# Kernel tuning notes

Hardware: AMD Instinct MI355X
Metric: run time of the kernel (lower is better)

Reference implementation:

```python
import jax, jax.numpy as jnp
import numpy as np

H, C = 16, 5           # GAT heads, per-head out channels
SIZE = 500             # max_pool_x size (time bins)
GAT_SLOPE, ACT_SLOPE = 0.2, 0.01


def _lrelu(x, s):
    return jnp.where(x >= 0, x, s * x)


def _gat(x, src, dst, ea, mask, W, We, a_s, a_d, a_e, b):
    # PyG GATConv: shared src/dst lin, edge_dim, self-loops already appended by caller
    N = x.shape[0]
    xp = (x @ W.T).reshape(N, H, C)                                   # [N,H,C]
    al = (jnp.einsum('nhc,hc->nh', xp, a_s)[src]
          + jnp.einsum('nhc,hc->nh', xp, a_d)[dst]
          + jnp.einsum('ehc,hc->eh', (ea @ We.T).reshape(-1, H, C), a_e))  # [E,H]
    al = _lrelu(al, GAT_SLOPE)
    if mask is not None:  # masked-out edges contribute nothing (equivalent to edge removal)
        al = jnp.where(mask[:, None], al, -jnp.inf)
    m = jax.ops.segment_max(al, dst, num_segments=N)                  # finite: every node has a self-loop
    e = jnp.exp(al - m[dst])
    coef = e / jax.ops.segment_sum(e, dst, num_segments=N)[dst]       # segment softmax over incoming edges
    out = jax.ops.segment_sum(coef[:, :, None] * xp[src], dst, num_segments=N)
    return out.reshape(N, H * C) + b


def _conv(x, w, b):
    y = jax.lax.conv_general_dilated(x, w, (2,), [(1, 1)],
                                     dimension_numbers=('NCH', 'OIH', 'NCH'))
    return y + b[None, :, None]


def _mlp(z, w1, b1, w2, b2, w3, b3):
    z = _lrelu(z @ w1.T + b1, ACT_SLOPE)
    z = _lrelu(z @ w2.T + b2, ACT_SLOPE)
    return z @ w3.T + b3


def _forward(x, edge_attr,
             gat1_W, gat1_We, gat1_as, gat1_ad, gat1_ae, gat1_b,
             gat2_W, gat2_We, gat2_as, gat2_ad, gat2_ae, gat2_b,
             conv1_w, conv1_b, conv2_w, conv2_b, conv3_w, conv3_b,
             chi_w1, chi_b1, chi_w2, chi_b2, chi_w3, chi_b3,
             rp_w1, rp_b1, rp_w2, rp_b2, rp_w3, rp_b3,
             t0_w1, t0_b1, t0_w2, t0_b2, t0_w3, t0_b3,
             edge_index, num_graphs):
    N = x.shape[0]
    loops = jnp.arange(N, dtype=edge_index.dtype)
    src = jnp.concatenate([edge_index[0], loops])
    dst = jnp.concatenate([edge_index[1], loops])
    ea = jnp.concatenate([edge_attr, jnp.zeros((N, edge_attr.shape[1]), edge_attr.dtype)], axis=0)
    timing = x[:, 2].astype(jnp.int32)   # non-differentiable, like .to(torch.long)

    h = _gat(x, src, dst, ea, None, gat1_W, gat1_We, gat1_as, gat1_ad, gat1_ae, gat1_b)
    mask2 = jnp.concatenate([edge_attr[:, 0] > 1.0, jnp.ones((N,), bool)])  # EdgeV[:,0]>1 + self loops
    h = _gat(h, src, dst, ea, mask2, gat2_W, gat2_We, gat2_as, gat2_ad, gat2_ae, gat2_b)

    # max_pool_x(cluster=Timing, batch, size=500): scatter-max into B*500 slots,
    # empty slots -> 0 (torch_scatter semantics); then view(-1, 80, 500)
    pooled = jax.ops.segment_max(h, timing, num_segments=num_graphs * SIZE)
    pooled = jnp.where(jnp.isfinite(pooled), pooled, 0.0)
    z = pooled.reshape(num_graphs, H * C, SIZE)

    z = _lrelu(_conv(z, conv1_w, conv1_b), ACT_SLOPE)   # [B,16,247]
    z = _lrelu(_conv(z, conv2_w, conv2_b), ACT_SLOPE)   # [B,16,120]
    z = _lrelu(_conv(z, conv3_w, conv3_b), ACT_SLOPE)   # [B,16,57]
    L = z.shape[-1]
    nw = (L - 10) // 10 + 1                              # MaxPool1d(k=10,s=10) -> 5
    z = z[..., :nw * 10].reshape(z.shape[0], z.shape[1], nw, 10).max(-1)
    z = z.reshape(z.shape[0], -1)                        # [B,80]

    chi0 = jnp.tanh(_mlp(z, chi_w1, chi_b1, chi_w2, chi_b2, chi_w3, chi_b3))
    rp = _mlp(z, rp_w1, rp_b1, rp_w2, rp_b2, rp_w3, rp_b3)
    t0 = _mlp(z, t0_w1, t0_b1, t0_w2, t0_b2, t0_w3, t0_b3)
    return jnp.concatenate([chi0, rp, t0], axis=1)       # [B,3]


def setup_inputs() -> dict:
    key = jax.random.key(0)
    ki = iter(jax.random.split(key, 50))
    N, E, B = 100_000, 1_200_000, 64
    x = jax.random.normal(next(ki), (N, 5), jnp.float32)
    timing = jax.random.randint(next(ki), (N,), 0, SIZE)
    x = x.at[:, 2].set(timing.astype(jnp.float32))       # Timing column holds integer bins
    src = jax.random.randint(next(ki), (E,), 0, N, dtype=jnp.int32)
    off = jax.random.randint(next(ki), (E,), 1, N, dtype=jnp.int32)
    dst = (src + off) % N                                # no pre-existing self-loops (PyG strips them)
    edge_index = jnp.stack([src, dst])
    edge_attr = jax.random.uniform(next(ki), (E, 2), jnp.float32) * 3.0  # ~2/3 pass col0>1 mask
    batch = jnp.sort(jax.random.randint(next(ki), (N,), 0, B, dtype=jnp.int32))

    def p(shape, scale=0.1):
        return jax.random.normal(next(ki), shape, jnp.float32) * scale

    return dict(
        x=x, edge_attr=edge_attr,
        gat1_W=p((80, 5)), gat1_We=p((80, 2)), gat1_as=p((16, 5)), gat1_ad=p((16, 5)), gat1_ae=p((16, 5)), gat1_b=p((80,)),
        gat2_W=p((80, 80)), gat2_We=p((80, 2)), gat2_as=p((16, 5)), gat2_ad=p((16, 5)), gat2_ae=p((16, 5)), gat2_b=p((80,)),
        conv1_w=p((16, 80, 10)), conv1_b=p((16,)),
        conv2_w=p((16, 16, 10)), conv2_b=p((16,)),
        conv3_w=p((16, 16, 10)), conv3_b=p((16,)),
        chi_w1=p((128, 80)), chi_b1=p((128,)), chi_w2=p((128, 128)), chi_b2=p((128,)), chi_w3=p((1, 128)), chi_b3=p((1,)),
        rp_w1=p((128, 80)), rp_b1=p((128,)), rp_w2=p((128, 128)), rp_b2=p((128,)), rp_w3=p((1, 128)), rp_b3=p((1,)),
        t0_w1=p((128, 80)), t0_b1=p((128,)), t0_w2=p((128, 128)), t0_b2=p((128,)), t0_w3=p((1, 128)), t0_b3=p((1,)),
        edge_index=edge_index, batch=batch, num_graphs=B)


def reference(x, edge_attr,
              gat1_W, gat1_We, gat1_as, gat1_ad, gat1_ae, gat1_b,
              gat2_W, gat2_We, gat2_as, gat2_ad, gat2_ae, gat2_b,
              conv1_w, conv1_b, conv2_w, conv2_b, conv3_w, conv3_b,
              chi_w1, chi_b1, chi_w2, chi_b2, chi_w3, chi_b3,
              rp_w1, rp_b1, rp_w2, rp_b2, rp_w3, rp_b3,
              t0_w1, t0_b1, t0_w2, t0_b2, t0_w3, t0_b3,
              edge_index, batch, num_graphs):
    del batch  # only used in torch to compute batch_size (passed here as num_graphs)
    return _forward(x, edge_attr,
                    gat1_W, gat1_We, gat1_as, gat1_ad, gat1_ae, gat1_b,
                    gat2_W, gat2_We, gat2_as, gat2_ad, gat2_ae, gat2_b,
                    conv1_w, conv1_b, conv2_w, conv2_b, conv3_w, conv3_b,
                    chi_w1, chi_b1, chi_w2, chi_b2, chi_w3, chi_b3,
                    rp_w1, rp_b1, rp_w2, rp_b2, rp_w3, rp_b3,
                    t0_w1, t0_b1, t0_w2, t0_b2, t0_w3, t0_b3,
                    edge_index, num_graphs)
```

## Files before the change

### kernel.cpp

```cpp
#include <hip/hip_runtime.h>
#include <math.h>

#define DEV static __device__ __forceinline__

DEV unsigned fenc(float f) {
    unsigned u = __float_as_uint(f);
    return (u & 0x80000000u) ? ~u : (u | 0x80000000u);
}
DEV float fdec(unsigned u) {
    return __uint_as_float((u & 0x80000000u) ? (u ^ 0x80000000u) : ~u);
}
DEV void atomic_max_u32(unsigned* p, unsigned v) {
    __hip_atomic_fetch_max(p, v, __ATOMIC_RELAXED, __HIP_MEMORY_SCOPE_AGENT);
}
DEV unsigned bf16(float f) {
    unsigned u = __float_as_uint(f);
    return (u + 0x7FFFu + ((u >> 16) & 1u)) >> 16;
}
DEV float unbf16(unsigned s) { return __uint_as_float(s << 16); }

__global__ void k_proj5t(const float* __restrict__ x, const float* __restrict__ W,
                         const float* __restrict__ a_s, const float* __restrict__ a_d,
                         unsigned short* __restrict__ xpb, float* __restrict__ dterm, int N) {
    int i = blockIdx.x * blockDim.x + threadIdx.x;
    if (i >= N * 16) return;
    int n = i >> 4, h = i & 15;
    float xr[5];
    #pragma unroll
    for (int j = 0; j < 5; ++j) xr[j] = x[(size_t)n * 5 + j];
    float o[5];
    #pragma unroll
    for (int c = 0; c < 5; ++c) {
        const float* wr = W + (size_t)(h * 5 + c) * 5;
        float s = 0.f;
        #pragma unroll
        for (int j = 0; j < 5; ++j) s += xr[j] * wr[j];
        o[c] = s;
    }
    float ss = 0.f, sd = 0.f;
    #pragma unroll
    for (int c = 0; c < 5; ++c) { ss += o[c] * a_s[h * 5 + c]; sd += o[c] * a_d[h * 5 + c]; }
    unsigned* p = (unsigned*)(xpb + (size_t)n * 96 + h * 6);
    p[0] = bf16(o[0]) | (bf16(o[1]) << 16);
    p[1] = bf16(o[2]) | (bf16(o[3]) << 16);
    p[2] = bf16(o[4]) | (bf16(ss) << 16);
    dterm[i] = sd;
}

__global__ __launch_bounds__(256) void k_proj80t(
    const unsigned short* __restrict__ in,
    const float* __restrict__ W,
    const float* __restrict__ a_s, const float* __restrict__ a_d,
    unsigned short* __restrict__ xpb, float* __restrict__ dterm, int N) {
    __shared__ float XS[16 * 136];
    __shared__ float WS[16 * 81];
    int tid = threadIdx.x;
    int n0 = blockIdx.x * 128;
    int h = tid & 15, ng = tid >> 4;

    float acc[8][5];
    #pragma unroll
    for (int j = 0; j < 8; ++j)
        #pragma unroll
        for (int c = 0; c < 5; ++c) acc[j][c] = 0.f;

    for (int k0 = 0; k0 < 80; k0 += 16) {
        __syncthreads();
        {
            int r = tid >> 1;
            int halfk = (tid & 1) * 8;
            int n = n0 + r; if (n >= N) n = N - 1;
            const uint4 v = *(const uint4*)(in + (size_t)n * 80 + k0 + halfk);
            unsigned uu[4] = {v.x, v.y, v.z, v.w};
            #pragma unroll
            for (int j = 0; j < 4; ++j) {
                XS[(halfk + 2 * j)     * 136 + r] = unbf16(uu[j] & 0xffff);
                XS[(halfk + 2 * j + 1) * 136 + r] = unbf16(uu[j] >> 16);
            }
        }
        {
            #pragma unroll
            for (int i = 0; i < 5; ++i) {
                int j = tid + i * 256;
                int oc = j >> 4, kk = j & 15;
                WS[kk * 81 + oc] = W[(size_t)oc * 80 + k0 + kk];
            }
        }
        __syncthreads();
        #pragma unroll
        for (int kk = 0; kk < 16; ++kk) {
            float4 xa = *(const float4*)&XS[kk * 136 + ng * 8];
            float4 xb = *(const float4*)&XS[kk * 136 + ng * 8 + 4];
            float wv[5];
            #pragma unroll
            for (int c = 0; c < 5; ++c) wv[c] = WS[kk * 81 + h * 5 + c];
            float xv[8] = {xa.x, xa.y, xa.z, xa.w, xb.x, xb.y, xb.z, xb.w};
            #pragma unroll
            for (int j = 0; j < 8; ++j)
                #pragma unroll
                for (int c = 0; c < 5; ++c) acc[j][c] += xv[j] * wv[c];
        }
    }
    float as_[5], ad_[5];
    #pragma unroll
    for (int c = 0; c < 5; ++c) { as_[c] = a_s[h * 5 + c]; ad_[c] = a_d[h * 5 + c]; }
    #pragma unroll
    for (int j = 0; j < 8; ++j) {
        int n = n0 + ng * 8 + j;
        if (n < N) {
            float ss = 0.f, sd = 0.f;
            #pragma unroll
            for (int c = 0; c < 5; ++c) { ss += acc[j][c] * as_[c]; sd += acc[j][c] * ad_[c]; }
            unsigned* p = (unsigned*)(xpb + (size_t)n * 96 + h * 6);
            p[0] = bf16(acc[j][0]) | (bf16(acc[j][1]) << 16);
            p[1] = bf16(acc[j][2]) | (bf16(acc[j][3]) << 16);
            p[2] = bf16(acc[j][4]) | (bf16(ss) << 16);
            dterm[n * 16 + h] = sd;
        }
    }
}

#define BIN_TILE 4096
__global__ __launch_bounds__(256) void k_cnt512(const int* __restrict__ dst,
        int* __restrict__ bcnt, int E, int NB) {
    __shared__ int cnt[512];
    int tid = threadIdx.x;
    for (int b = tid; b < NB; b += 256) cnt[b] = 0;
    __syncthreads();
    int e0 = blockIdx.x * BIN_TILE;
    #pragma unroll
    for (int k = 0; k < BIN_TILE / 256; ++k) {
        int e = e0 + k * 256 + tid;
        if (e < E) atomicAdd(&cnt[((unsigned)dst[e]) >> 8], 1);
    }
    __syncthreads();
    for (int b = tid; b < NB; b += 256) {
        int c = cnt[b];
        if (c) __hip_atomic_fetch_add(&bcnt[b], c, __ATOMIC_RELAXED, __HIP_MEMORY_SCOPE_AGENT);
    }
}

__global__ void k_scan512(const int* __restrict__ bcnt, int* __restrict__ boff,
                          int* __restrict__ bcur, int* __restrict__ off,
                          int NB, int N, int E) {
    __shared__ int sm[512];
    int t = threadIdx.x;
    int v = (t < NB) ? bcnt[t] : 0;
    sm[t] = v;
    __syncthreads();
    for (int s = 1; s < 512; s <<= 1) {
        int u = (t >= s) ? sm[t - s] : 0;
        __syncthreads();
        sm[t] += u;
        __syncthreads();
    }
    int excl = sm[t] - v;
    if (t < NB) { boff[t] = excl; bcur[t] = excl; }
    if (t == NB - 1) boff[NB] = excl + v;
    if (t == 0) off[N] = E;
}

__global__ __launch_bounds__(256) void k_bin(const int* __restrict__ src,
        const int* __restrict__ dst, const float* __restrict__ ea,
        int* __restrict__ bcur, uint4* __restrict__ ebuf, int E, int NB) {
    __shared__ int cnt[512];
    __shared__ int base[512];
    int tid = threadIdx.x;
    for (int b = tid; b < NB; b += 256) cnt[b] = 0;
    __syncthreads();
    int e0 = blockIdx.x * BIN_TILE;
    #pragma unroll
    for (int k = 0; k < BIN_TILE / 256; ++k) {
        int e = e0 + k * 256 + tid;
        if (e < E) atomicAdd(&cnt[((unsigned)dst[e]) >> 8], 1);
    }
    __syncthreads();
    for (int b = tid; b < NB; b += 256) {
        int c = cnt[b];
        base[b] = c ? __hip_atomic_fetch_add(&bcur[b], c, __ATOMIC_RELAXED,
                                             __HIP_MEMORY_SCOPE_AGENT) : 0;
        cnt[b] = 0;
    }
    __syncthreads();
    #pragma unroll
    for (int k = 0; k < BIN_TILE / 256; ++k) {
        int e = e0 + k * 256 + tid;
        if (e < E) {
            int d = dst[e];
            int b = ((unsigned)d) >> 8;
            int r = atomicAdd(&cnt[b], 1);
            float a0 = ea[2 * e], a1 = ea[2 * e + 1];
            unsigned s = (unsigned)src[e] | (a0 > 1.0f ? 0x80000000u : 0u);
            ebuf[base[b] + r] = make_uint4(s, bf16(a0) | (bf16(a1) << 16), (unsigned)d, 0u);
        }
    }
}

__global__ __launch_bounds__(256) void k_perm2(const int* __restrict__ boff,
        const uint4* __restrict__ ebuf, uint2* __restrict__ erec,
        int* __restrict__ off, int N) {
    __shared__ int cnt[256];
    __shared__ int sm[256];
    int b = blockIdx.x, tid = threadIdx.x;
    int d0 = b << 8;
    int s0 = boff[b], s1 = boff[b + 1];
    cnt[tid] = 0;
    __syncthreads();
    for (int i = s0 + tid; i < s1; i += 256)
        atomicAdd(&cnt[(int)ebuf[i].z - d0], 1);
    __syncthreads();
    int v = cnt[tid];
    sm[tid] = v;
    __syncthreads();
    for (int s = 1; s < 256; s <<= 1) {
        int u = (tid >= s) ? sm[tid - s] : 0;
        __syncthreads();
        sm[tid] += u;
        __syncthreads();
    }
    int excl = sm[tid] - v;
    if (d0 + tid < N) off[d0 + tid] = s0 + excl;
    cnt[tid] = s0 + excl;
    __syncthreads();
    for (int i = s0 + tid; i < s1; i += 256) {
        uint4 r = ebuf[i];
        int p = atomicAdd(&cnt[(int)r.z - d0], 1);
        erec[p] = make_uint2(r.x, r.y);
    }
}

template<bool MASKED, bool OUT_BF16>
__global__ void k_gat(const int* __restrict__ off, const uint2* __restrict__ erec,
                      const float* __restrict__ dterm,
                      const float* __restrict__ We, const float* __restrict__ a_e,
                      const unsigned short* __restrict__ xpb,
                      const float* __restrict__ bias, void* __restrict__ hout, int N) {
    int i = blockIdx.x * blockDim.x + threadIdx.x;
    if (i >= N * 16) return;
    int d = i >> 4, h = i & 15;
    float q0 = 0.f, q1 = 0.f;
    #pragma unroll
    for (int c = 0; c < 5; ++c) {
        float ae = a_e[h * 5 + c];
        q0 += We[(h * 5 + c) * 2 + 0] * ae;
        q1 += We[(h * 5 + c) * 2 + 1] * ae;
    }
    float dt = dterm[i];
    int e0 = off[d], e1 = off[d + 1];

    float m, den = 1.f, n0, n1, n2, n3, n4;
    {
        const uint3 v = *(const uint3*)(xpb + (size_t)d * 96 + h * 6);
        n0 = unbf16(v.x & 0xffff); n1 = unbf16(v.x >> 16);
        n2 = unbf16(v.y & 0xffff); n3 = unbf16(v.y >> 16);
        n4 = unbf16(v.z & 0xffff);
        float sl = unbf16(v.z >> 16) + dt;
        m = fmaxf(sl, 0.2f * sl);
    }

    uint2 r_cur = make_uint2(0, 0), r_nxt = make_uint2(0, 0);
    uint3 v_cur = make_uint3(0, 0, 0), v_nxt = make_uint3(0, 0, 0);
    if (e0 < e1) {
        r_cur = erec[e0];
        if (!MASKED || (r_cur.x >> 31))
            v_cur = *(const uint3*)(xpb + (size_t)(r_cur.x & 0x7fffffff) * 96 + h * 6);
    }
    if (e0 + 1 < e1) r_nxt = erec[e0 + 1];
    for (int e = e0; e < e1; ++e) {
        uint2 r_n2 = make_uint2(0, 0);
        if (e + 2 < e1) r_n2 = erec[e + 2];
        if (e + 1 < e1 && (!MASKED || (r_nxt.x >> 31)))
            v_nxt = *(const uint3*)(xpb + (size_t)(r_nxt.x & 0x7fffffff) * 96 + h * 6);
        bool keep = !MASKED || (r_cur.x >> 31);
        if (keep) {
            float ea0 = unbf16(r_cur.y & 0xffff), ea1 = unbf16(r_cur.y >> 16);
            uint3 v = v_cur;
            float st = unbf16(v.z >> 16);
            float al = st + dt + ea0 * q0 + ea1 * q1;
            al = fmaxf(al, 0.2f * al);
            float x0 = unbf16(v.x & 0xffff), x1 = unbf16(v.x >> 16);
            float x2 = unbf16(v.y & 0xffff), x3 = unbf16(v.y >> 16);
            float x4 = unbf16(v.z & 0xffff);
            bool gt = al > m;
            float t = __expf(-fabsf(al - m));
            float c = gt ? t : 1.f;
            float w = gt ? 1.f : t;
            m = fmaxf(m, al);
            den = den * c + w;
            n0 = n0 * c + w * x0;
            n1 = n1 * c + w * x1;
            n2 = n2 * c + w * x2;
            n3 = n3 * c + w * x3;
            n4 = n4 * c + w * x4;
        }
        r_cur = r_nxt; r_nxt = r_n2; v_cur = v_nxt;
    }
    float inv = 1.0f / den;
    const float* br = bias + h * 5;
    float v0 = n0 * inv + br[0];
    float v1 = n1 * inv + br[1];
    float v2 = n2 * inv + br[2];
    float v3 = n3 * inv + br[3];
    float v4 = n4 * inv + br[4];
    if (OUT_BF16) {
        unsigned short* orow = (unsigned short*)hout + (size_t)d * 80 + h * 5;
        orow[0] = (unsigned short)bf16(v0);
        orow[1] = (unsigned short)bf16(v1);
        orow[2] = (unsigned short)bf16(v2);
        orow[3] = (unsigned short)bf16(v3);
        orow[4] = (unsigned short)bf16(v4);
    } else {
        float* orow = (float*)hout + (size_t)d * 80 + h * 5;
        orow[0] = v0; orow[1] = v1; orow[2] = v2; orow[3] = v3; orow[4] = v4;
    }
}

__global__ void k_pool8(const float* __restrict__ x, const unsigned short* __restrict__ h2b,
                        unsigned* __restrict__ psl, int N) {
    int i = blockIdx.x * blockDim.x + threadIdx.x;
    if (i >= N * 80) return;
    int n = i / 80, ch = i % 80;
    int t = (int)x[(size_t)n * 5 + 2];
    unsigned* slice = psl + (size_t)(blockIdx.x & 7) * 40000;
    atomic_max_u32(&slice[t * 80 + ch], fenc(unbf16(h2b[i])));
}

__global__ void k_poolred(const unsigned* __restrict__ psl, float* __restrict__ pool) {
    int i = blockIdx.x * blockDim.x + threadIdx.x;
    if (i >= 40000) return;
    unsigned m = 0u;
    #pragma unroll
    for (int s = 0; s < 8; ++s) m = max(m, psl[s * 40000 + i]);
    pool[i] = (m == 0u) ? 0.f : fdec(m);
}

__global__ __launch_bounds__(256) void k_conv1(const float* __restrict__ pool,
        const float* __restrict__ w, const float* __restrict__ b,
        float* __restrict__ c1) {
    __shared__ float XS[80 * 44];
    __shared__ float WS[16 * 972];
    int gg = blockIdx.x >> 4, chunk = blockIdx.x & 15;
    int t0 = chunk * 16;
    int tid = threadIdx.x;
    for (int idx = tid; idx < 80 * 44; idx += 256) {
        int ic = idx / 44, j = idx % 44;
        int p = 2 * t0 - 1 + j;
        XS[idx] = (gg == 0 && j < 41 && p >= 0 && p < 500) ? pool[ic * 500 + p] : 0.f;
    }
    for (int idx = tid; idx < 12800; idx += 256) {
        int oc = idx / 800, r = idx % 800;
        int ic = r / 10, k = r % 10;
        WS[oc * 972 + ic * 12 + k] = w[idx];
    }
    __syncthreads();
    int oc = tid >> 4, tg = tid & 15;
    float acc = 0.f;
    for (int ic = 0; ic < 80; ++ic) {
        const float* xr = &XS[ic * 44 + 2 * tg];
        const float* wr = &WS[oc * 972 + ic * 12];
        #pragma unroll
        for (int k = 0; k < 10; ++k) acc += xr[k] * wr[k];
    }
    int t = t0 + tg;
    if (t < 247) {
        float s = acc + b[oc];
        c1[(size_t)gg * 3952 + oc * 247 + t] = s >= 0.f ? s : 0.01f * s;
    }
}

__global__ __launch_bounds__(128) void k_conv2(const float* __restrict__ c1,
        const float* __restrict__ w2c, const float* __restrict__ b2c,
        float* __restrict__ c2g) {
    __shared__ float Z1[16 * 248];
    __shared__ float WS[160];
    int g = blockIdx.x >> 4, oc = blockIdx.x & 15;
    int tid = threadIdx.x;
    for (int idx = tid; idx < 16 * 247; idx += 128) {
        int ic = idx / 247, t = idx % 247;
        Z1[ic * 248 + t] = c1[(size_t)g * 3952 + idx];
    }
    for (int idx = tid; idx < 160; idx += 128) WS[idx] = w2c[oc * 160 + idx];
    __syncthreads();
    if (tid < 120) {
        float s = b2c[oc];
        #pragma unroll 4
        for (int ic = 0; ic < 16; ++ic) {
            const float* xr = &Z1[ic * 248];
            const float* wr = &WS[ic * 10];
            #pragma unroll
            for (int k = 0; k < 10; ++k) {
                int p = 2 * tid + k - 1;
                if (p >= 0 && p < 247) s += xr[p] * wr[k];
            }
        }
        c2g[g * 1920 + oc * 120 + tid] = s >= 0.f ? s : 0.01f * s;
    }
}

__global__ __launch_bounds__(128) void k_conv3(const float* __restrict__ c2g,
        const float* __restrict__ w3c, const float* __restrict__ b3c,
        float* __restrict__ c3g) {
    __shared__ float Z2[16 * 121];
    __shared__ float WS[160];
    int g = blockIdx.x >> 4, oc = blockIdx.x & 15;
    int tid = threadIdx.x;
    for (int idx = tid; idx < 16 * 120; idx += 128) {
        int ic = idx / 120, t = idx % 120;
        Z2[ic * 121 + t] = c2g[g * 1920 + idx];
    }
    for (int idx = tid; idx < 160; idx += 128) WS[idx] = w3c[oc * 160 + idx];
    __syncthreads();
    if (tid < 57) {
        float s = b3c[oc];
        #pragma unroll 4
        for (int ic = 0; ic < 16; ++ic) {
            const float* xr = &Z2[ic * 121];
            const float* wr = &WS[ic * 10];
            #pragma unroll
            for (int k = 0; k < 10; ++k) {
                int p = 2 * tid + k - 1;
                if (p >= 0 && p < 120) s += xr[p] * wr[k];
            }
        }
        c3g[g * 912 + oc * 57 + tid] = s >= 0.f ? s : 0.01f * s;
    }
}

struct HeadW { const float *w1, *b1, *w2, *b2, *w3, *b3; };

__global__ __launch_bounds__(128) void k_heads(const float* __restrict__ c3g,
        HeadW hw0, HeadW hw1, HeadW hw2, float* __restrict__ out, int B) {
    __shared__ float Z3[16 * 57];
    __shared__ float ZF[80], HB[128], HC[128];
    __shared__ float partial[2];
    __shared__ float oval;
    int g = blockIdx.x / 3, hd = blockIdx.x % 3;
    int tid = threadIdx.x;
    const HeadW hw = (hd == 0) ? hw0 : (hd == 1) ? hw1 : hw2;
    for (int idx = tid; idx < 912; idx += 128) Z3[idx] = c3g[g * 912 + idx];
    __syncthreads();
    if (tid < 80) {
        int ch = tid / 5, wd = tid % 5;
        const float* p = &Z3[ch * 57 + wd * 10];
        float m = p[0];
        #pragma unroll
        for (int k = 1; k < 10; ++k) m = fmaxf(m, p[k]);
        ZF[tid] = m;
    }
    __syncthreads();
    float s = hw.b1[tid];
    for (int k = 0; k < 80; ++k) s += ZF[k] * hw.w1[tid * 80 + k];
    HB[tid] = s >= 0.f ? s : 0.01f * s;
    __syncthreads();
    s = hw.b2[tid];
    for (int k = 0; k < 128; ++k) s += HB[k] * hw.w2[tid * 128 + k];
    HC[tid] = s >= 0.f ? s : 0.01f * s;
    __syncthreads();
    float p = HC[tid] * hw.w3[tid];
    #pragma unroll
    for (int o = 32; o > 0; o >>= 1) p += __shfl_down(p, o, 64);
    if ((tid & 63) == 0) partial[tid >> 6] = p;
    __syncthreads();
    if (tid == 0) {
        float o = partial[0] + partial[1] + hw.b3[0];
        o = (hd == 0) ? tanhf(o) : o;
        oval = o;
        if (g == 0) out[hd] = o;
    }
    __syncthreads();
    if (g == 1) {
        float o = oval;
        for (int gg = 1 + tid; gg < B; gg += 128) out[gg * 3 + hd] = o;
    }
}

extern "C" void kernel_launch(void* const* d_in, const int* in_sizes, int n_in,
                              void* d_out, int out_size, void* d_ws, size_t ws_size,
                              hipStream_t stream) {
    const float* x     = (const float*)d_in[0];
    const float* ea    = (const float*)d_in[1];
    const float* g1_W  = (const float*)d_in[2];
    const float* g1_We = (const float*)d_in[3];
    const float* g1_as = (const float*)d_in[4];
    const float* g1_ad = (const float*)d_in[5];
    const float* g1_ae = (const float*)d_in[6];
    const float* g1_b  = (const float*)d_in[7];
    const float* g2_W  = (const float*)d_in[8];
    const float* g2_We = (const float*)d_in[9];
    const float* g2_as = (const float*)d_in[10];
    const float* g2_ad = (const float*)d_in[11];
    const float* g2_ae = (const float*)d_in[12];
    const float* g2_b  = (const float*)d_in[13];
    const float* c1w = (const float*)d_in[14]; const float* c1b = (const float*)d_in[15];
    const float* c2w = (const float*)d_in[16]; const float* c2b = (const float*)d_in[17];
    const float* c3w = (const float*)d_in[18]; const float* c3b = (const float*)d_in[19];
    const int*   eidx = (const int*)d_in[38];
    float* out = (float*)d_out;

    const int N = in_sizes[0] / 5;
    const int E = in_sizes[38] / 2;
    const int B = out_size / 3;
    const int* src = eidx;
    const int* dst = eidx + E;

    float* ws = (float*)d_ws;
    size_t o = 0;
    auto alloc = [&](size_t n) { float* p = ws + o; o = (o + n + 3) & ~(size_t)3; return p; };
    unsigned short* xpb = (unsigned short*)alloc((size_t)N * 48);
    float*    Hbuf  = alloc((size_t)N * 80);
    float*    dterm = alloc((size_t)N * 16);
    int*      off   = (int*)alloc((size_t)N + 1);
    int*      bcnt  = (int*)alloc(512);
    int*      boff  = (int*)alloc(516);
    int*      bcur  = (int*)alloc(512);
    uint4*    ebuf  = (uint4*)alloc((size_t)E * 4);
    uint2*    erec  = (uint2*)alloc((size_t)E * 2);
    unsigned* psl   = (unsigned*)alloc(8 * 40000);
    float*    pool  = alloc(40000);
    float*    c1    = alloc(2 * 3952);
    float*    c2g   = alloc(2 * 1920);
    float*    c3g   = alloc(2 * 912);

    const int BS = 256;
    auto blocks = [&](long long n) { return (int)((n + BS - 1) / BS); };
    const int NB = (N + 255) / 256;
    const int TILES = (E + BIN_TILE - 1) / BIN_TILE;

    hipMemsetAsync(bcnt, 0, 512 * 4, stream);
    hipMemsetAsync(psl, 0, 8 * 40000 * 4, stream);
    k_cnt512<<<TILES, 256, 0, stream>>>(dst, bcnt, E, NB);
    k_scan512<<<1, 512, 0, stream>>>(bcnt, boff, bcur, off, NB, N, E);
    k_bin<<<TILES, 256, 0, stream>>>(src, dst, ea, bcur, ebuf, E, NB);
    k_perm2<<<NB, 256, 0, stream>>>(boff, ebuf, erec, off, N);

    k_proj5t<<<blocks((long long)N * 16), BS, 0, stream>>>(x, g1_W, g1_as, g1_ad,
                                                           xpb, dterm, N);
    k_gat<false, true><<<blocks((long long)N * 16), BS, 0, stream>>>(
        off, erec, dterm, g1_We, g1_ae, xpb, g1_b, (void*)Hbuf, N);

    k_proj80t<<<(N + 127) / 128, 256, 0, stream>>>((const unsigned short*)Hbuf, g2_W,
                                                   g2_as, g2_ad, xpb, dterm, N);
    k_gat<true, true><<<blocks((long long)N * 16), BS, 0, stream>>>(
        off, erec, dterm, g2_We, g2_ae, xpb, g2_b, (void*)Hbuf, N);

    k_pool8<<<blocks((long long)N * 80), BS, 0, stream>>>(x, (const unsigned short*)Hbuf,
                                                          psl, N);
    k_poolred<<<blocks(40000), BS, 0, stream>>>(psl, pool);

    k_conv1<<<32, 256, 0, stream>>>(pool, c1w, c1b, c1);
    k_conv2<<<32, 128, 0, stream>>>(c1, c2w, c2b, c2g);
    k_conv3<<<32, 128, 0, stream>>>(c2g, c3w, c3b, c3g);
    HeadW h0 = {(const float*)d_in[20], (const float*)d_in[21], (const float*)d_in[22],
                (const float*)d_in[23], (const float*)d_in[24], (const float*)d_in[25]};
    HeadW h1 = {(const float*)d_in[26], (const float*)d_in[27], (const float*)d_in[28],
                (const float*)d_in[29], (const float*)d_in[30], (const float*)d_in[31]};
    HeadW h2 = {(const float*)d_in[32], (const float*)d_in[33], (const float*)d_in[34],
                (const float*)d_in[35], (const float*)d_in[36], (const float*)d_in[37]};
    k_heads<<<6, 128, 0, stream>>>(c3g, h0, h1, h2, out, B);
}
```

Before: 416.2 us.

## Build compacted masked-edge CSR for second GAT and fuse pool reduction into conv1

Counts and scatters the masked edges (ea0>1) into a second CSR so the second GAT layer walks only the surviving edges, with no per-edge branch. It also stores source row offsets premultiplied by the row stride and pads erec, which lets the GAT loop drop its bounds checks. The pool-slice max reduction moves into conv1's tile load, removing the k_poolred kernel. The cost is extra atomics, scans and memory traffic in the binning kernels, and conv1 now does redundant slice reads.

```diff
diff --git a/kernel.cpp b/kernel.cpp
--- a/kernel.cpp
+++ b/kernel.cpp
@@ -122,42 +122,53 @@
 
 #define BIN_TILE 4096
 __global__ __launch_bounds__(256) void k_cnt512(const int* __restrict__ dst,
-        int* __restrict__ bcnt, int E, int NB) {
-    __shared__ int cnt[512];
-    int tid = threadIdx.x;
-    for (int b = tid; b < NB; b += 256) cnt[b] = 0;
+        const float* __restrict__ ea, int* __restrict__ bcnt, int E, int NB) {
+    __shared__ int cnt[512], cnt2[512];
+    int tid = threadIdx.x;
+    for (int b = tid; b < NB; b += 256) { cnt[b] = 0; cnt2[b] = 0; }
     __syncthreads();
     int e0 = blockIdx.x * BIN_TILE;
     #pragma unroll
     for (int k = 0; k < BIN_TILE / 256; ++k) {
         int e = e0 + k * 256 + tid;
-        if (e < E) atomicAdd(&cnt[((unsigned)dst[e]) >> 8], 1);
+        if (e < E) {
+            int b = ((unsigned)dst[e]) >> 8;
+            atomicAdd(&cnt[b], 1);
+            if (ea[2 * e] > 1.0f) atomicAdd(&cnt2[b], 1);
+        }
     }
     __syncthreads();
     for (int b = tid; b < NB; b += 256) {
-        int c = cnt[b];
-        if (c) __hip_atomic_fetch_add(&bcnt[b], c, __ATOMIC_RELAXED, __HIP_MEMORY_SCOPE_AGENT);
-    }
-}
-
-__global__ void k_scan512(const int* __restrict__ bcnt, int* __restrict__ boff,
-                          int* __restrict__ bcur, int* __restrict__ off,
-                          int NB, int N, int E) {
-    __shared__ int sm[512];
+        if (cnt[b])  __hip_atomic_fetch_add(&bcnt[b], cnt[b], __ATOMIC_RELAXED, __HIP_MEMORY_SCOPE_AGENT);
+        if (cnt2[b]) __hip_atomic_fetch_add(&bcnt[512 + b], cnt2[b], __ATOMIC_RELAXED, __HIP_MEMORY_SCOPE_AGENT);
+    }
+}
+
+__global__ void k_scan512(const int* __restrict__ bcnt,
+        int* __restrict__ boff, int* __restrict__ bcur, int* __restrict__ boff2,
+        int* __restrict__ off, int* __restrict__ off2,
+        uint2* __restrict__ erec, uint2* __restrict__ erec2, int NB, int N, int E) {
+    __shared__ int sm[512], sm2[512];
     int t = threadIdx.x;
-    int v = (t < NB) ? bcnt[t] : 0;
-    sm[t] = v;
+    int v  = (t < NB) ? bcnt[t] : 0;
+    int v2 = (t < NB) ? bcnt[512 + t] : 0;
+    sm[t] = v; sm2[t] = v2;
     __syncthreads();
     for (int s = 1; s < 512; s <<= 1) {
-        int u = (t >= s) ? sm[t - s] : 0;
+        int u = (t >= s) ? sm[t - s] : 0, u2 = (t >= s) ? sm2[t - s] : 0;
         __syncthreads();
-        sm[t] += u;
+        sm[t] += u; sm2[t] += u2;
         __syncthreads();
     }
-    int excl = sm[t] - v;
-    if (t < NB) { boff[t] = excl; bcur[t] = excl; }
-    if (t == NB - 1) boff[NB] = excl + v;
-    if (t == 0) off[N] = E;
+    int excl = sm[t] - v, excl2 = sm2[t] - v2;
+    if (t < NB) { boff[t] = excl; bcur[t] = excl; boff2[t] = excl2; }
+    if (t == NB - 1) {
+        int K = excl2 + v2;
+        boff[NB] = excl + v; boff2[NB] = K;
+        erec[E] = make_uint2(0, 0);  erec[E + 1] = make_uint2(0, 0);
+        erec2[K] = make_uint2(0, 0); erec2[K + 1] = make_uint2(0, 0);
+        off[N] = E; off2[N] = K;
+    }
 }
 
 __global__ __launch_bounds__(256) void k_bin(const int* __restrict__ src,
@@ -190,51 +201,63 @@
             int b = ((unsigned)d) >> 8;
             int r = atomicAdd(&cnt[b], 1);
             float a0 = ea[2 * e], a1 = ea[2 * e + 1];
-            unsigned s = (unsigned)src[e] | (a0 > 1.0f ? 0x80000000u : 0u);
-            ebuf[base[b] + r] = make_uint4(s, bf16(a0) | (bf16(a1) << 16), (unsigned)d, 0u);
+            unsigned ro = (unsigned)src[e] * 192u;
+            if (a0 > 1.0f) ro |= 0x80000000u;
+            ebuf[base[b] + r] = make_uint4(ro, bf16(a0) | (bf16(a1) << 16), (unsigned)d, 0u);
         }
     }
 }
 
 __global__ __launch_bounds__(256) void k_perm2(const int* __restrict__ boff,
-        const uint4* __restrict__ ebuf, uint2* __restrict__ erec,
-        int* __restrict__ off, int N) {
-    __shared__ int cnt[256];
-    __shared__ int sm[256];
+        const int* __restrict__ boff2, const uint4* __restrict__ ebuf,
+        uint2* __restrict__ erec, uint2* __restrict__ erec2,
+        int* __restrict__ off, int* __restrict__ off2, int N) {
+    __shared__ int cA[256], sA[256], cB[256], sB[256];
     int b = blockIdx.x, tid = threadIdx.x;
     int d0 = b << 8;
     int s0 = boff[b], s1 = boff[b + 1];
-    cnt[tid] = 0;
-    __syncthreads();
-    for (int i = s0 + tid; i < s1; i += 256)
-        atomicAdd(&cnt[(int)ebuf[i].z - d0], 1);
-    __syncthreads();
-    int v = cnt[tid];
-    sm[tid] = v;
-    __syncthreads();
-    for (int s = 1; s < 256; s <<= 1) {
-        int u = (tid >= s) ? sm[tid - s] : 0;
-        __syncthreads();
-        sm[tid] += u;
-        __syncthreads();
-    }
-    int excl = sm[tid] - v;
-    if (d0 + tid < N) off[d0 + tid] = s0 + excl;
-    cnt[tid] = s0 + excl;
+    int s20 = boff2[b];
+    cA[tid] = 0; cB[tid] = 0;
     __syncthreads();
     for (int i = s0 + tid; i < s1; i += 256) {
         uint4 r = ebuf[i];
-        int p = atomicAdd(&cnt[(int)r.z - d0], 1);
-        erec[p] = make_uint2(r.x, r.y);
-    }
-}
-
-template<bool MASKED, bool OUT_BF16>
+        int l = (int)r.z - d0;
+        atomicAdd(&cA[l], 1);
+        if (r.x >> 31) atomicAdd(&cB[l], 1);
+    }
+    __syncthreads();
+    int vA = cA[tid], vB = cB[tid];
+    sA[tid] = vA; sB[tid] = vB;
+    __syncthreads();
+    for (int s = 1; s < 256; s <<= 1) {
+        int uA = (tid >= s) ? sA[tid - s] : 0, uB = (tid >= s) ? sB[tid - s] : 0;
+        __syncthreads();
+        sA[tid] += uA; sB[tid] += uB;
+        __syncthreads();
+    }
+    int eA = sA[tid] - vA, eB = sB[tid] - vB;
+    if (d0 + tid < N) { off[d0 + tid] = s0 + eA; off2[d0 + tid] = s20 + eB; }
+    cA[tid] = s0 + eA; cB[tid] = s20 + eB;
+    __syncthreads();
+    for (int i = s0 + tid; i < s1; i += 256) {
+        uint4 r = ebuf[i];
+        int l = (int)r.z - d0;
+        unsigned ro = r.x & 0x7fffffffu;
+        int p = atomicAdd(&cA[l], 1);
+        erec[p] = make_uint2(ro, r.y);
+        if (r.x >> 31) {
+            int p2 = atomicAdd(&cB[l], 1);
+            erec2[p2] = make_uint2(ro, r.y);
+        }
+    }
+}
+
 __global__ void k_gat(const int* __restrict__ off, const uint2* __restrict__ erec,
                       const float* __restrict__ dterm,
                       const float* __restrict__ We, const float* __restrict__ a_e,
                       const unsigned short* __restrict__ xpb,
-                      const float* __restrict__ bias, void* __restrict__ hout, int N) {
+                      const float* __restrict__ bias, unsigned short* __restrict__ hout,
+                      int N) {
     int i = blockIdx.x * blockDim.x + threadIdx.x;
     if (i >= N * 16) return;
     int d = i >> 4, h = i & 15;
@@ -246,11 +269,12 @@
         q1 += We[(h * 5 + c) * 2 + 1] * ae;
     }
     float dt = dterm[i];
-    int e0 = off[d], e1 = off[d + 1];
+    const char* xb = (const char*)xpb;
+    int hoff = h * 12;
 
     float m, den = 1.f, n0, n1, n2, n3, n4;
     {
-        const uint3 v = *(const uint3*)(xpb + (size_t)d * 96 + h * 6);
+        const uint3 v = *(const uint3*)(xb + d * 192 + hoff);
         n0 = unbf16(v.x & 0xffff); n1 = unbf16(v.x >> 16);
         n2 = unbf16(v.y & 0xffff); n3 = unbf16(v.y >> 16);
         n4 = unbf16(v.z & 0xffff);
@@ -258,61 +282,42 @@
         m = fmaxf(sl, 0.2f * sl);
     }
 
-    uint2 r_cur = make_uint2(0, 0), r_nxt = make_uint2(0, 0);
-    uint3 v_cur = make_uint3(0, 0, 0), v_nxt = make_uint3(0, 0, 0);
-    if (e0 < e1) {
-        r_cur = erec[e0];
-        if (!MASKED || (r_cur.x >> 31))
-            v_cur = *(const uint3*)(xpb + (size_t)(r_cur.x & 0x7fffffff) * 96 + h * 6);
-    }
-    if (e0 + 1 < e1) r_nxt = erec[e0 + 1];
+    int e0 = off[d], e1 = off[d + 1];
+    uint2 r_cur = erec[e0];
+    uint2 r_nxt = erec[e0 + 1];
+    uint3 v_cur = *(const uint3*)(xb + r_cur.x + hoff);
     for (int e = e0; e < e1; ++e) {
-        uint2 r_n2 = make_uint2(0, 0);
-        if (e + 2 < e1) r_n2 = erec[e + 2];
-        if (e + 1 < e1 && (!MASKED || (r_nxt.x >> 31)))
-            v_nxt = *(const uint3*)(xpb + (size_t)(r_nxt.x & 0x7fffffff) * 96 + h * 6);
-        bool keep = !MASKED || (r_cur.x >> 31);
-        if (keep) {
-            float ea0 = unbf16(r_cur.y & 0xffff), ea1 = unbf16(r_cur.y >> 16);
-            uint3 v = v_cur;
-            float st = unbf16(v.z >> 16);
-            float al = st + dt + ea0 * q0 + ea1 * q1;
-            al = fmaxf(al, 0.2f * al);
-            float x0 = unbf16(v.x & 0xffff), x1 = unbf16(v.x >> 16);
-            float x2 = unbf16(v.y & 0xffff), x3 = unbf16(v.y >> 16);
-            float x4 = unbf16(v.z & 0xffff);
-            bool gt = al > m;
-            float t = __expf(-fabsf(al - m));
-            float c = gt ? t : 1.f;
-            float w = gt ? 1.f : t;
-            m = fmaxf(m, al);
-            den = den * c + w;
-            n0 = n0 * c + w * x0;
-            n1 = n1 * c + w * x1;
-            n2 = n2 * c + w * x2;
-            n3 = n3 * c + w * x3;
-            n4 = n4 * c + w * x4;
-        }
-        r_cur = r_nxt; r_nxt = r_n2; v_cur = v_nxt;
+        uint2 r_n2 = erec[e + 2];
+        uint3 v_n  = *(const uint3*)(xb + r_nxt.x + hoff);
+        float ea0 = unbf16(r_cur.y & 0xffff), ea1 = unbf16(r_cur.y >> 16);
+        uint3 v = v_cur;
+        float st = unbf16(v.z >> 16);
+        float al = st + dt + ea0 * q0 + ea1 * q1;
+        al = fmaxf(al, 0.2f * al);
+        float x0 = unbf16(v.x & 0xffff), x1 = unbf16(v.x >> 16);
+        float x2 = unbf16(v.y & 0xffff), x3 = unbf16(v.y >> 16);
+        float x4 = unbf16(v.z & 0xffff);
+        bool gt = al > m;
+        float t = __expf(-fabsf(al - m));
+        float c = gt ? t : 1.f;
+        float w = gt ? 1.f : t;
+        m = fmaxf(m, al);
+        den = den * c + w;
+        n0 = n0 * c + w * x0;
+        n1 = n1 * c + w * x1;
+        n2 = n2 * c + w * x2;
+        n3 = n3 * c + w * x3;
+        n4 = n4 * c + w * x4;
+        r_cur = r_nxt; r_nxt = r_n2; v_cur = v_n;
     }
     float inv = 1.0f / den;
     const float* br = bias + h * 5;
-    float v0 = n0 * inv + br[0];
-    float v1 = n1 * inv + br[1];
-    float v2 = n2 * inv + br[2];
-    float v3 = n3 * inv + br[3];
-    float v4 = n4 * inv + br[4];
-    if (OUT_BF16) {
-        unsigned short* orow = (unsigned short*)hout + (size_t)d * 80 + h * 5;
-        orow[0] = (unsigned short)bf16(v0);
-        orow[1] = (unsigned short)bf16(v1);
-        orow[2] = (unsigned short)bf16(v2);
-        orow[3] = (unsigned short)bf16(v3);
-        orow[4] = (unsigned short)bf16(v4);
-    } else {
-        float* orow = (float*)hout + (size_t)d * 80 + h * 5;
-        orow[0] = v0; orow[1] = v1; orow[2] = v2; orow[3] = v3; orow[4] = v4;
-    }
+    unsigned short* orow = hout + (size_t)d * 80 + h * 5;
+    orow[0] = (unsigned short)bf16(n0 * inv + br[0]);
+    orow[1] = (unsigned short)bf16(n1 * inv + br[1]);
+    orow[2] = (unsigned short)bf16(n2 * inv + br[2]);
+    orow[3] = (unsigned short)bf16(n3 * inv + br[3]);
+    orow[4] = (unsigned short)bf16(n4 * inv + br[4]);
 }
 
 __global__ void k_pool8(const float* __restrict__ x, const unsigned short* __restrict__ h2b,
@@ -325,16 +330,7 @@
     atomic_max_u32(&slice[t * 80 + ch], fenc(unbf16(h2b[i])));
 }
 
-__global__ void k_poolred(const unsigned* __restrict__ psl, float* __restrict__ pool) {
-    int i = blockIdx.x * blockDim.x + threadIdx.x;
-    if (i >= 40000) return;
-    unsigned m = 0u;
-    #pragma unroll
-    for (int s = 0; s < 8; ++s) m = max(m, psl[s * 40000 + i]);
-    pool[i] = (m == 0u) ? 0.f : fdec(m);
-}
-
-__global__ __launch_bounds__(256) void k_conv1(const float* __restrict__ pool,
+__global__ __launch_bounds__(256) void k_conv1(const unsigned* __restrict__ psl,
         const float* __restrict__ w, const float* __restrict__ b,
         float* __restrict__ c1) {
     __shared__ float XS[80 * 44];
@@ -345,7 +341,15 @@
     for (int idx = tid; idx < 80 * 44; idx += 256) {
         int ic = idx / 44, j = idx % 44;
         int p = 2 * t0 - 1 + j;
-        XS[idx] = (gg == 0 && j < 41 && p >= 0 && p < 500) ? pool[ic * 500 + p] : 0.f;
+        float v = 0.f;
+        if (gg == 0 && j < 41 && p >= 0 && p < 500) {
+            int jf = ic * 500 + p;
+            unsigned u = 0u;
+            #pragma unroll
+            for (int s = 0; s < 8; ++s) u = max(u, psl[s * 40000 + jf]);
+            v = (u == 0u) ? 0.f : fdec(u);
+        }
+        XS[idx] = v;
     }
     for (int idx = tid; idx < 12800; idx += 256) {
         int oc = idx / 800, r = idx % 800;
@@ -510,13 +514,15 @@
     float*    Hbuf  = alloc((size_t)N * 80);
     float*    dterm = alloc((size_t)N * 16);
     int*      off   = (int*)alloc((size_t)N + 1);
-    int*      bcnt  = (int*)alloc(512);
+    int*      off2  = (int*)alloc((size_t)N + 1);
+    int*      bcnt  = (int*)alloc(1024);
     int*      boff  = (int*)alloc(516);
+    int*      boff2 = (int*)alloc(516);
     int*      bcur  = (int*)alloc(512);
     uint4*    ebuf  = (uint4*)alloc((size_t)E * 4);
-    uint2*    erec  = (uint2*)alloc((size_t)E * 2);
+    uint2*    erec  = (uint2*)alloc((size_t)(E + 2) * 2);
+    uint2*    erec2 = (uint2*)alloc((size_t)(E + 2) * 2);
     unsigned* psl   = (unsigned*)alloc(8 * 40000);
-    float*    pool  = alloc(40000);
     float*    c1    = alloc(2 * 3952);
     float*    c2g   = alloc(2 * 1920);
     float*    c3g   = alloc(2 * 912);
@@ -526,28 +532,28 @@
     const int NB = (N + 255) / 256;
     const int TILES = (E + BIN_TILE - 1) / BIN_TILE;
 
-    hipMemsetAsync(bcnt, 0, 512 * 4, stream);
+    hipMemsetAsync(bcnt, 0, 1024 * 4, stream);
     hipMemsetAsync(psl, 0, 8 * 40000 * 4, stream);
-    k_cnt512<<<TILES, 256, 0, stream>>>(dst, bcnt, E, NB);
-    k_scan512<<<1, 512, 0, stream>>>(bcnt, boff, bcur, off, NB, N, E);
+    k_cnt512<<<TILES, 256, 0, stream>>>(dst, ea, bcnt, E, NB);
+    k_scan512<<<1, 512, 0, stream>>>(bcnt, boff, bcur, boff2, off, off2,
+                                     erec, erec2, NB, N, E);
     k_bin<<<TILES, 256, 0, stream>>>(src, dst, ea, bcur, ebuf, E, NB);
-    k_perm2<<<NB, 256, 0, stream>>>(boff, ebuf, erec, off, N);
+    k_perm2<<<NB, 256, 0, stream>>>(boff, boff2, ebuf, erec, erec2, off, off2, N);
 
     k_proj5t<<<blocks((long long)N * 16), BS, 0, stream>>>(x, g1_W, g1_as, g1_ad,
                                                            xpb, dterm, N);
-    k_gat<false, true><<<blocks((long long)N * 16), BS, 0, stream>>>(
-        off, erec, dterm, g1_We, g1_ae, xpb, g1_b, (void*)Hbuf, N);
+    k_gat<<<blocks((long long)N * 16), BS, 0, stream>>>(
+        off, erec, dterm, g1_We, g1_ae, xpb, g1_b, (unsigned short*)Hbuf, N);
 
     k_proj80t<<<(N + 127) / 128, 256, 0, stream>>>((const unsigned short*)Hbuf, g2_W,
                                                    g2_as, g2_ad, xpb, dterm, N);
-    k_gat<true, true><<<blocks((long long)N * 16), BS, 0, stream>>>(
-        off, erec, dterm, g2_We, g2_ae, xpb, g2_b, (void*)Hbuf, N);
+    k_gat<<<blocks((long long)N * 16), BS, 0, stream>>>(
+        off2, erec2, dterm, g2_We, g2_ae, xpb, g2_b, (unsigned short*)Hbuf, N);
 
     k_pool8<<<blocks((long long)N * 80), BS, 0, stream>>>(x, (const unsigned short*)Hbuf,
                                                           psl, N);
-    k_poolred<<<blocks(40000), BS, 0, stream>>>(psl, pool);
-
-    k_conv1<<<32, 256, 0, stream>>>(pool, c1w, c1b, c1);
+
+    k_conv1<<<32, 256, 0, stream>>>(psl, c1w, c1b, c1);
     k_conv2<<<32, 128, 0, stream>>>(c1, c2w, c2b, c2g);
     k_conv3<<<32, 128, 0, stream>>>(c2g, c3w, c3b, c3g);
     HeadW h0 = {(const float*)d_in[20], (const float*)d_in[21], (const float*)d_in[22],
```

Result: no change. 411.0 us (-1.3%).
